# Kernel optimization log

Measured on AMD Instinct MI355X. Metric: run time of the kernel, lower is better.

## Reference

```python
import jax, jax.numpy as jnp
import numpy as np

EMBED = 2048
HEAD = 128

def setup_inputs() -> dict:
    key = jax.random.key(0)
    ks = jax.random.split(key, 7)
    s = 1.0 / np.sqrt(EMBED)
    x = jax.random.normal(ks[0], (8, 2048, EMBED), dtype=jnp.float32)
    Wq = jax.random.uniform(ks[1], (EMBED, HEAD), jnp.float32, -s, s)
    bq = jax.random.uniform(ks[2], (HEAD,), jnp.float32, -s, s)
    Wk = jax.random.uniform(ks[3], (EMBED, HEAD), jnp.float32, -s, s)
    bk = jax.random.uniform(ks[4], (HEAD,), jnp.float32, -s, s)
    Wv = jax.random.uniform(ks[5], (EMBED, HEAD), jnp.float32, -s, s)
    bv = jax.random.uniform(ks[6], (HEAD,), jnp.float32, -s, s)
    return {"x": x, "Wq": Wq, "bq": bq, "Wk": Wk, "bk": bk, "Wv": Wv, "bv": bv}

def reference(x, Wq, bq, Wk, bk, Wv, bv):
    # x: [B, T, E]
    T = x.shape[1]
    Q = x @ Wq + bq  # [B, T, H]
    K = x @ Wk + bk
    V = x @ Wv + bv
    scale = 1.0 / jnp.sqrt(jnp.float32(HEAD))
    scores = jnp.einsum('bqh,bkh->bqk', Q, K) * scale  # [B, T, T]
    causal = jnp.tril(jnp.ones((T, T), dtype=bool))
    scores = jnp.where(causal, scores, jnp.float32(-jnp.inf))
    att = jax.nn.softmax(scores, axis=-1)
    # dropout is identity in eval/reference mode
    return jnp.einsum('bqk,bkh->bqh', att, V)
```

## Files before the change

### kernel.cpp

```cpp
#include <hip/hip_runtime.h>

#define EMBED 2048
#define HEAD 128
#define BATCH 8
#define SEQ 2048

typedef __attribute__((ext_vector_type(4))) float f32x4;
typedef __attribute__((ext_vector_type(8))) __bf16 bf16x8;
typedef __attribute__((ext_vector_type(8))) short short8;

static __device__ __forceinline__ ushort f2bf(float x){
    unsigned u = __float_as_uint(x);
    u += 0x7fffu + ((u >> 16) & 1u);
    return (ushort)(u >> 16);
}

#define MFMA16(a,b,c) __builtin_amdgcn_mfma_f32_16x16x32_bf16((a),(b),(c),0,0,0)

#define GLL16(g, l) __builtin_amdgcn_global_load_lds( \
    (const __attribute__((address_space(1))) void*)(g), \
    (__attribute__((address_space(3))) void*)(l), 16, 0, 0)

__global__ __launch_bounds__(256) void prep_wt(const float* __restrict__ Wq,
                                               const float* __restrict__ Wk,
                                               const float* __restrict__ Wv,
                                               ushort* __restrict__ wt){
    __shared__ float ld[64][129];
    const int w  = blockIdx.y;
    const int k0 = blockIdx.x * 64;
    const int tid = threadIdx.x;
    const float* W = (w == 0) ? Wq : ((w == 1) ? Wk : Wv);
    #pragma unroll
    for (int ii = 0; ii < 32; ii++){
        int idx = tid + 256 * ii;
        int row = idx >> 7, col = idx & 127;
        ld[row][col] = W[(size_t)(k0 + row) * HEAD + col];
    }
    __syncthreads();
    int n  = tid >> 1;
    int kh = (tid & 1) * 32;
    __attribute__((aligned(16))) ushort tmp[32];
    #pragma unroll
    for (int ii = 0; ii < 32; ii++) tmp[ii] = f2bf(ld[kh + ii][n]);
    ushort* dst = wt + (size_t)(w * HEAD + n) * EMBED + k0 + kh;
    #pragma unroll
    for (int q = 0; q < 4; q++)
        *(short8*)(dst + q * 8) = *(const short8*)(tmp + q * 8);
}

__global__ __launch_bounds__(256) void qkv_gemm(const float* __restrict__ x,
                                                const ushort* __restrict__ wt,
                                                const float* __restrict__ bq,
                                                const float* __restrict__ bk,
                                                const float* __restrict__ bv,
                                                ushort* __restrict__ Qb,
                                                ushort* __restrict__ Kb,
                                                ushort* __restrict__ Vt){
    __shared__ char smem[51200];
    float* ts = (float*)smem;

    const int nt    = blockIdx.x;
    const int mtile = blockIdx.y;
    const int tid   = threadIdx.x;
    const int lane  = tid & 63;
    const int wid   = tid >> 6;
    const int l15   = lane & 15, lhi = lane >> 4;
    const int wm    = wid >> 1,  wn  = wid & 1;
    const int xrow0 = mtile * 64;

    const int srow = tid >> 3;
    const int ssub = tid & 7;

    const ushort* wtn = wt + (size_t)(nt * HEAD) * EMBED;
    const int grow = lane >> 3;
    const int gch  = lane & 7;

    f32x4 acc[2][4];
    #pragma unroll
    for (int i = 0; i < 2; i++)
        #pragma unroll
        for (int j = 0; j < 4; j++) acc[i][j] = (f32x4){0.f,0.f,0.f,0.f};

    float4 xr[2][2];
    const int NK = EMBED / 64;

    {
        const float* xp = x + (size_t)xrow0 * EMBED;
        #pragma unroll
        for (int h = 0; h < 2; h++){
            xr[h][0] = *(const float4*)(xp + (size_t)(srow + 32*h) * EMBED + ssub * 8);
            xr[h][1] = *(const float4*)(xp + (size_t)(srow + 32*h) * EMBED + ssub * 8 + 4);
        }
        #pragma unroll
        for (int g = 0; g < 4; g++){
            int r0  = wid * 32 + g * 8;
            int row = r0 + grow;
            GLL16(wtn + (size_t)row * EMBED + ((gch ^ grow) * 8), smem + 18432 + r0 * 128);
        }
        #pragma unroll
        for (int h = 0; h < 2; h++){
            __attribute__((aligned(16))) ushort t8[8];
            t8[0]=f2bf(xr[h][0].x); t8[1]=f2bf(xr[h][0].y); t8[2]=f2bf(xr[h][0].z); t8[3]=f2bf(xr[h][0].w);
            t8[4]=f2bf(xr[h][1].x); t8[5]=f2bf(xr[h][1].y); t8[6]=f2bf(xr[h][1].z); t8[7]=f2bf(xr[h][1].w);
            *(short8*)(smem + (srow + 32*h) * 144 + ssub * 16) = *(const short8*)t8;
        }
    }
    __syncthreads();

    int cur = 0;
    for (int kt = 0; kt < NK; ++kt){
        char* xsb_c = smem + cur * 9216;
        char* wlb_c = smem + 18432 + cur * 16384;
        char* xsb_n = smem + (cur ^ 1) * 9216;
        char* wlb_n = smem + 18432 + (cur ^ 1) * 16384;
        if (kt < NK - 1){
            const float* xp = x + (size_t)xrow0 * EMBED + (kt + 1) * 64;
            #pragma unroll
            for (int h = 0; h < 2; h++){
                xr[h][0] = *(const float4*)(xp + (size_t)(srow + 32*h) * EMBED + ssub * 8);
                xr[h][1] = *(const float4*)(xp + (size_t)(srow + 32*h) * EMBED + ssub * 8 + 4);
            }
            const ushort* wsrc = wtn + (kt + 1) * 64;
            #pragma unroll
            for (int g = 0; g < 4; g++){
                int r0  = wid * 32 + g * 8;
                int row = r0 + grow;
                GLL16(wsrc + (size_t)row * EMBED + ((gch ^ grow) * 8), wlb_n + r0 * 128);
            }
        }
        #pragma unroll
        for (int kc = 0; kc < 2; kc++){
            bf16x8 af[2], bfj[4];
            #pragma unroll
            for (int i = 0; i < 2; i++)
                af[i] = *(const bf16x8*)(xsb_c + (wm*32 + i*16 + l15) * 144 + kc*64 + lhi*16);
            #pragma unroll
            for (int j = 0; j < 4; j++){
                int row = wn*64 + j*16 + l15;
                bfj[j] = *(const bf16x8*)(wlb_c + row * 128 + (((kc*4 + lhi) ^ (l15 & 7)) * 16));
            }
            #pragma unroll
            for (int i = 0; i < 2; i++)
                #pragma unroll
                for (int j = 0; j < 4; j++)
                    acc[i][j] = MFMA16(af[i], bfj[j], acc[i][j]);
        }
        if (kt < NK - 1){
            #pragma unroll
            for (int h = 0; h < 2; h++){
                __attribute__((aligned(16))) ushort t8[8];
                t8[0]=f2bf(xr[h][0].x); t8[1]=f2bf(xr[h][0].y); t8[2]=f2bf(xr[h][0].z); t8[3]=f2bf(xr[h][0].w);
                t8[4]=f2bf(xr[h][1].x); t8[5]=f2bf(xr[h][1].y); t8[6]=f2bf(xr[h][1].z); t8[7]=f2bf(xr[h][1].w);
                *(short8*)(xsb_n + (srow + 32*h) * 144 + ssub * 16) = *(const short8*)t8;
            }
        }
        __syncthreads();
        cur ^= 1;
    }

    const float* bias = (nt == 0) ? bq : ((nt == 1) ? bk : bv);
    float bval[4];
    #pragma unroll
    for (int j = 0; j < 4; j++) bval[j] = bias[wn*64 + j*16 + l15];

    if (nt < 2){
        ushort* dst = (nt == 0) ? Qb : Kb;
        #pragma unroll
        for (int i = 0; i < 2; i++)
            #pragma unroll
            for (int j = 0; j < 4; j++)
                #pragma unroll
                for (int r = 0; r < 4; r++){
                    int m = mtile*64 + wm*32 + i*16 + lhi*4 + r;
                    int c = wn*64 + j*16 + l15;
                    dst[(size_t)m * HEAD + c] = f2bf(acc[i][j][r] + bval[j]);
                }
    } else {
        __syncthreads();
        #pragma unroll
        for (int i = 0; i < 2; i++)
            #pragma unroll
            for (int j = 0; j < 4; j++)
                #pragma unroll
                for (int r = 0; r < 4; r++){
                    int ml = wm*32 + i*16 + lhi*4 + r;
                    int c  = wn*64 + j*16 + l15;
                    ts[ml * 132 + c] = acc[i][j][r] + bval[j];
                }
        __syncthreads();
        int n  = tid >> 1;
        int mc = (tid & 1) * 32;
        int bb = mtile >> 5;
        int trow = (mtile & 31) * 64 + mc;
        __attribute__((aligned(16))) ushort tmp[32];
        #pragma unroll
        for (int ii = 0; ii < 32; ii++) tmp[ii] = f2bf(ts[(mc + ii) * 132 + n]);
        ushort* dst = Vt + ((size_t)(bb * HEAD + n)) * SEQ + trow;
        #pragma unroll
        for (int q = 0; q < 4; q++)
            *(short8*)(dst + q * 8) = *(const short8*)(tmp + q * 8);
    }
}

__global__ __launch_bounds__(256) void attn(const ushort* __restrict__ Qb,
                                            const ushort* __restrict__ Kb,
                                            const ushort* __restrict__ Vt,
                                            float* __restrict__ po,
                                            float* __restrict__ pm,
                                            float* __restrict__ pl){
    __shared__ char smem[40960];
    char* Ks = smem;
    char* Vs = smem + 16384;
    char* Ps = smem + 32768;

    const int slot = blockIdx.x;
    const int b    = blockIdx.y;
    const int qi   = slot >> 1;
    const int qt   = (b < 4) ? qi : (31 - qi);
    const int half = slot & 1;
    const int NT   = qt + 1;
    const int tmid = (NT + 1) >> 1;
    const int t0   = half ? tmid : 0;
    const int t1   = half ? NT : tmid;

    const int qb    = qt * 64;
    const int tid   = threadIdx.x;
    const int lane  = tid & 63, wid = tid >> 6;
    const int l15   = lane & 15, lhi = lane >> 4;
    const float scale = 0.08838834764831845f;

    bf16x8 qf[4];
    {
        const ushort* qp = Qb + ((size_t)(b * SEQ + qb + wid * 16 + l15)) * HEAD;
        #pragma unroll
        for (int kc = 0; kc < 4; kc++)
            qf[kc] = *(const bf16x8*)(qp + kc * 32 + lhi * 8);
    }

    f32x4 o[8];
    #pragma unroll
    for (int d = 0; d < 8; d++) o[d] = (f32x4){0.f,0.f,0.f,0.f};
    float mr[4] = {-1e30f,-1e30f,-1e30f,-1e30f};
    float lr[4] = {0.f,0.f,0.f,0.f};

    char* Pw = Ps + wid * 2048;

    const int krow = tid >> 4, kch = tid & 15;
    const int vd   = tid >> 3, vch = tid & 7;

    short8 kr[4], vr[4];
    {
        const int kvb = t0 * 64;
        #pragma unroll
        for (int j = 0; j < 4; j++)
            kr[j] = *(const short8*)(Kb + ((size_t)(b * SEQ + kvb + krow + 16*j)) * HEAD + kch * 8);
        #pragma unroll
        for (int j = 0; j < 4; j++)
            vr[j] = *(const short8*)(Vt + ((size_t)(b * HEAD + vd + 32*j)) * SEQ + kvb + vch * 8);
    }

    for (int t = t0; t < t1; ++t){
        __syncthreads();
        #pragma unroll
        for (int j = 0; j < 4; j++){
            int row = krow + 16*j;
            *(short8*)(Ks + row * 256 + ((kch ^ (row & 15)) * 16)) = kr[j];
        }
        #pragma unroll
        for (int j = 0; j < 4; j++){
            int d = vd + 32*j;
            *(short8*)(Vs + d * 128 + ((vch ^ (d & 7)) * 16)) = vr[j];
        }
        if (t + 1 < t1){
            const int kvb2 = (t + 1) * 64;
            #pragma unroll
            for (int j = 0; j < 4; j++)
                kr[j] = *(const short8*)(Kb + ((size_t)(b * SEQ + kvb2 + krow + 16*j)) * HEAD + kch * 8);
            #pragma unroll
            for (int j = 0; j < 4; j++)
                vr[j] = *(const short8*)(Vt + ((size_t)(b * HEAD + vd + 32*j)) * SEQ + kvb2 + vch * 8);
        }
        asm volatile("s_waitcnt lgkmcnt(0)" ::: "memory");
        __builtin_amdgcn_s_barrier();
        __builtin_amdgcn_sched_barrier(0);

        const int kvb = t * 64;
        f32x4 s[4];
        #pragma unroll
        for (int ns = 0; ns < 4; ns++){
            s[ns] = (f32x4){0.f,0.f,0.f,0.f};
            int row = ns * 16 + l15;
            #pragma unroll
            for (int kc = 0; kc < 4; kc++){
                int ch = (kc * 4 + lhi) ^ (row & 15);
                bf16x8 bfr = *(const bf16x8*)(Ks + row * 256 + ch * 16);
                s[ns] = MFMA16(qf[kc], bfr, s[ns]);
            }
        }

        float mx[4];
        #pragma unroll
        for (int r = 0; r < 4; r++){
            #pragma unroll
            for (int ns = 0; ns < 4; ns++){
                float v = s[ns][r] * scale;
                if (t == qt){
                    int kvg = kvb + ns * 16 + l15;
                    int qg  = qb + wid * 16 + lhi * 4 + r;
                    if (kvg > qg) v = -1e30f;
                }
                s[ns][r] = v;
            }
            float m0 = fmaxf(fmaxf(s[0][r], s[1][r]), fmaxf(s[2][r], s[3][r]));
            m0 = fmaxf(m0, __shfl_xor(m0, 1));
            m0 = fmaxf(m0, __shfl_xor(m0, 2));
            m0 = fmaxf(m0, __shfl_xor(m0, 4));
            m0 = fmaxf(m0, __shfl_xor(m0, 8));
            mx[r] = m0;
        }
        float alpha[4];
        #pragma unroll
        for (int r = 0; r < 4; r++){
            float mn = fmaxf(mr[r], mx[r]);
            alpha[r] = __expf(mr[r] - mn);
            mr[r] = mn;
            float sum = 0.f;
            #pragma unroll
            for (int ns = 0; ns < 4; ns++){
                float p = __expf(s[ns][r] - mn);
                s[ns][r] = p;
                sum += p;
            }
            sum += __shfl_xor(sum, 1);
            sum += __shfl_xor(sum, 2);
            sum += __shfl_xor(sum, 4);
            sum += __shfl_xor(sum, 8);
            lr[r] = lr[r] * alpha[r] + sum;
        }
        #pragma unroll
        for (int d = 0; d < 8; d++)
            #pragma unroll
            for (int r = 0; r < 4; r++) o[d][r] *= alpha[r];

        #pragma unroll
        for (int ns = 0; ns < 4; ns++)
            #pragma unroll
            for (int r = 0; r < 4; r++){
                int row = lhi * 4 + r;
                int byteoff = row * 128 + (((ns * 16 + l15) * 2) ^ ((row & 7) << 4));
                *(ushort*)(Pw + byteoff) = f2bf(s[ns][r]);
            }
        asm volatile("s_waitcnt lgkmcnt(0)" ::: "memory");
        __builtin_amdgcn_sched_barrier(0);

        #pragma unroll
        for (int kc = 0; kc < 2; kc++){
            int abyte = l15 * 128 + ((kc * 64 + lhi * 16) ^ ((l15 & 7) << 4));
            bf16x8 af = *(const bf16x8*)(Pw + abyte);
            #pragma unroll
            for (int ds = 0; ds < 8; ds++){
                int drow = ds * 16 + l15;
                int bbyte = drow * 128 + ((kc * 64 + lhi * 16) ^ ((drow & 7) << 4));
                bf16x8 bfr = *(const bf16x8*)(Vs + bbyte);
                o[ds] = MFMA16(af, bfr, o[ds]);
            }
        }
    }

    float* pob = po + ((size_t)half * 16384 + (size_t)b * SEQ) * HEAD;
    #pragma unroll
    for (int r = 0; r < 4; r++){
        int q = qb + wid * 16 + lhi * 4 + r;
        #pragma unroll
        for (int ds = 0; ds < 8; ds++)
            pob[(size_t)q * HEAD + ds * 16 + l15] = o[ds][r];
        if (l15 == 0){
            pm[half * 16384 + b * SEQ + q] = mr[r];
            pl[half * 16384 + b * SEQ + q] = lr[r];
        }
    }
}

__global__ __launch_bounds__(256) void merge(const float* __restrict__ po,
                                             const float* __restrict__ pm,
                                             const float* __restrict__ pl,
                                             float* __restrict__ out){
    int g = blockIdx.x * 256 + threadIdx.x;
    int row = g >> 2;
    int dq  = (g & 3) * 32;
    float m0 = pm[row], m1 = pm[16384 + row];
    float l0 = pl[row], l1 = pl[16384 + row];
    float M  = fmaxf(m0, m1);
    float w0 = __expf(m0 - M), w1 = __expf(m1 - M);
    float inv = 1.0f / (w0 * l0 + w1 * l1);
    const float4* p0 = (const float4*)(po + (size_t)row * HEAD + dq);
    const float4* p1 = (const float4*)(po + (size_t)(16384 + row) * HEAD + dq);
    float4* op = (float4*)(out + (size_t)row * HEAD + dq);
    #pragma unroll
    for (int i = 0; i < 8; i++){
        float4 a = p0[i], c = p1[i];
        float4 r;
        r.x = (w0*a.x + w1*c.x) * inv;
        r.y = (w0*a.y + w1*c.y) * inv;
        r.z = (w0*a.z + w1*c.z) * inv;
        r.w = (w0*a.w + w1*c.w) * inv;
        op[i] = r;
    }
}

extern "C" void kernel_launch(void* const* d_in, const int* in_sizes, int n_in,
                              void* d_out, int out_size, void* d_ws, size_t ws_size,
                              hipStream_t stream){
    const float* x  = (const float*)d_in[0];
    const float* Wq = (const float*)d_in[1];
    const float* bq = (const float*)d_in[2];
    const float* Wk = (const float*)d_in[3];
    const float* bk = (const float*)d_in[4];
    const float* Wv = (const float*)d_in[5];
    const float* bv = (const float*)d_in[6];
    float* out = (float*)d_out;

    char* ws = (char*)d_ws;
    ushort* Qb = (ushort*)ws;
    ushort* Kb = (ushort*)(ws + (size_t)4  * 1024 * 1024);
    ushort* Vt = (ushort*)(ws + (size_t)8  * 1024 * 1024);
    ushort* Wt = (ushort*)(ws + (size_t)12 * 1024 * 1024);
    float*  po = (float*) (ws + (size_t)14 * 1024 * 1024);
    float*  pm = (float*) (ws + (size_t)31 * 1024 * 1024);
    float*  pl = (float*) (ws + (size_t)31 * 1024 * 1024 + 262144);

    prep_wt <<<dim3(32, 3), 256, 0, stream>>>(Wq, Wk, Wv, Wt);
    qkv_gemm<<<dim3(3, 256), 256, 0, stream>>>(x, Wt, bq, bk, bv, Qb, Kb, Vt);
    attn    <<<dim3(64, 8), 256, 0, stream>>>(Qb, Kb, Vt, po, pm, pl);
    merge   <<<256, 256, 0, stream>>>(po, pm, pl, out);
}
```

Measured before the change: 115.0 us.

## Fuse Q/K/V projections into one block per row tile to read x once

Each QKV GEMM block now computes all 384 output columns (Q, K and V) for its 64-row tile, using 512 threads and 8 waves laid out 2x4, instead of launching three blocks per tile that each reload and re-convert the same x rows. This cuts the fp32 x global traffic and the bf16 conversion work by a factor of three. In exchange, LDS use grows to about 114 KB per block, which limits occupancy, and only 256 blocks are launched, which may underfill the GPU. The epilogue routes the column groups to Q, K or the transposed V buffer.

```diff
diff --git a/kernel.cpp b/kernel.cpp
--- a/kernel.cpp
+++ b/kernel.cpp
@@ -48,7 +48,7 @@
         *(short8*)(dst + q * 8) = *(const short8*)(tmp + q * 8);
 }
 
-__global__ __launch_bounds__(256) void qkv_gemm(const float* __restrict__ x,
+__global__ __launch_bounds__(512) void qkv_gemm(const float* __restrict__ x,
                                                 const ushort* __restrict__ wt,
                                                 const float* __restrict__ bq,
                                                 const float* __restrict__ bk,
@@ -56,149 +56,136 @@
                                                 ushort* __restrict__ Qb,
                                                 ushort* __restrict__ Kb,
                                                 ushort* __restrict__ Vt){
-    __shared__ char smem[51200];
+    __shared__ char smem[116736];
     float* ts = (float*)smem;
 
-    const int nt    = blockIdx.x;
-    const int mtile = blockIdx.y;
+    const int mtile = blockIdx.x;
     const int tid   = threadIdx.x;
     const int lane  = tid & 63;
     const int wid   = tid >> 6;
     const int l15   = lane & 15, lhi = lane >> 4;
-    const int wm    = wid >> 1,  wn  = wid & 1;
+    const int wm    = wid >> 2,  wn  = wid & 3;
     const int xrow0 = mtile * 64;
 
     const int srow = tid >> 3;
     const int ssub = tid & 7;
 
-    const ushort* wtn = wt + (size_t)(nt * HEAD) * EMBED;
     const int grow = lane >> 3;
     const int gch  = lane & 7;
 
-    f32x4 acc[2][4];
+    f32x4 acc[2][6];
     #pragma unroll
     for (int i = 0; i < 2; i++)
         #pragma unroll
-        for (int j = 0; j < 4; j++) acc[i][j] = (f32x4){0.f,0.f,0.f,0.f};
-
-    float4 xr[2][2];
+        for (int j = 0; j < 6; j++) acc[i][j] = (f32x4){0.f,0.f,0.f,0.f};
+
+    float4 xr0, xr1;
     const int NK = EMBED / 64;
 
     {
-        const float* xp = x + (size_t)xrow0 * EMBED;
-        #pragma unroll
-        for (int h = 0; h < 2; h++){
-            xr[h][0] = *(const float4*)(xp + (size_t)(srow + 32*h) * EMBED + ssub * 8);
-            xr[h][1] = *(const float4*)(xp + (size_t)(srow + 32*h) * EMBED + ssub * 8 + 4);
-        }
-        #pragma unroll
-        for (int g = 0; g < 4; g++){
-            int r0  = wid * 32 + g * 8;
+        const float* xp = x + (size_t)(xrow0 + srow) * EMBED;
+        xr0 = *(const float4*)(xp + ssub * 8);
+        xr1 = *(const float4*)(xp + ssub * 8 + 4);
+        #pragma unroll
+        for (int g = 0; g < 6; g++){
+            int r0  = wid * 48 + g * 8;
             int row = r0 + grow;
-            GLL16(wtn + (size_t)row * EMBED + ((gch ^ grow) * 8), smem + 18432 + r0 * 128);
-        }
-        #pragma unroll
-        for (int h = 0; h < 2; h++){
-            __attribute__((aligned(16))) ushort t8[8];
-            t8[0]=f2bf(xr[h][0].x); t8[1]=f2bf(xr[h][0].y); t8[2]=f2bf(xr[h][0].z); t8[3]=f2bf(xr[h][0].w);
-            t8[4]=f2bf(xr[h][1].x); t8[5]=f2bf(xr[h][1].y); t8[6]=f2bf(xr[h][1].z); t8[7]=f2bf(xr[h][1].w);
-            *(short8*)(smem + (srow + 32*h) * 144 + ssub * 16) = *(const short8*)t8;
-        }
+            GLL16(wt + (size_t)row * EMBED + ((gch ^ grow) * 8), smem + 18432 + r0 * 128);
+        }
+        __attribute__((aligned(16))) ushort t8[8];
+        t8[0]=f2bf(xr0.x); t8[1]=f2bf(xr0.y); t8[2]=f2bf(xr0.z); t8[3]=f2bf(xr0.w);
+        t8[4]=f2bf(xr1.x); t8[5]=f2bf(xr1.y); t8[6]=f2bf(xr1.z); t8[7]=f2bf(xr1.w);
+        *(short8*)(smem + srow * 144 + ssub * 16) = *(const short8*)t8;
     }
     __syncthreads();
 
     int cur = 0;
     for (int kt = 0; kt < NK; ++kt){
         char* xsb_c = smem + cur * 9216;
-        char* wlb_c = smem + 18432 + cur * 16384;
+        char* wlb_c = smem + 18432 + cur * 49152;
         char* xsb_n = smem + (cur ^ 1) * 9216;
-        char* wlb_n = smem + 18432 + (cur ^ 1) * 16384;
+        char* wlb_n = smem + 18432 + (cur ^ 1) * 49152;
         if (kt < NK - 1){
-            const float* xp = x + (size_t)xrow0 * EMBED + (kt + 1) * 64;
-            #pragma unroll
-            for (int h = 0; h < 2; h++){
-                xr[h][0] = *(const float4*)(xp + (size_t)(srow + 32*h) * EMBED + ssub * 8);
-                xr[h][1] = *(const float4*)(xp + (size_t)(srow + 32*h) * EMBED + ssub * 8 + 4);
-            }
-            const ushort* wsrc = wtn + (kt + 1) * 64;
-            #pragma unroll
-            for (int g = 0; g < 4; g++){
-                int r0  = wid * 32 + g * 8;
+            const float* xp = x + (size_t)(xrow0 + srow) * EMBED + (kt + 1) * 64;
+            xr0 = *(const float4*)(xp + ssub * 8);
+            xr1 = *(const float4*)(xp + ssub * 8 + 4);
+            const ushort* wsrc = wt + (kt + 1) * 64;
+            #pragma unroll
+            for (int g = 0; g < 6; g++){
+                int r0  = wid * 48 + g * 8;
                 int row = r0 + grow;
                 GLL16(wsrc + (size_t)row * EMBED + ((gch ^ grow) * 8), wlb_n + r0 * 128);
             }
         }
         #pragma unroll
         for (int kc = 0; kc < 2; kc++){
-            bf16x8 af[2], bfj[4];
+            bf16x8 af[2], bfj[6];
             #pragma unroll
             for (int i = 0; i < 2; i++)
                 af[i] = *(const bf16x8*)(xsb_c + (wm*32 + i*16 + l15) * 144 + kc*64 + lhi*16);
             #pragma unroll
-            for (int j = 0; j < 4; j++){
-                int row = wn*64 + j*16 + l15;
+            for (int j = 0; j < 6; j++){
+                int row = wn*96 + j*16 + l15;
                 bfj[j] = *(const bf16x8*)(wlb_c + row * 128 + (((kc*4 + lhi) ^ (l15 & 7)) * 16));
             }
             #pragma unroll
             for (int i = 0; i < 2; i++)
                 #pragma unroll
-                for (int j = 0; j < 4; j++)
+                for (int j = 0; j < 6; j++)
                     acc[i][j] = MFMA16(af[i], bfj[j], acc[i][j]);
         }
         if (kt < NK - 1){
-            #pragma unroll
-            for (int h = 0; h < 2; h++){
-                __attribute__((aligned(16))) ushort t8[8];
-                t8[0]=f2bf(xr[h][0].x); t8[1]=f2bf(xr[h][0].y); t8[2]=f2bf(xr[h][0].z); t8[3]=f2bf(xr[h][0].w);
-                t8[4]=f2bf(xr[h][1].x); t8[5]=f2bf(xr[h][1].y); t8[6]=f2bf(xr[h][1].z); t8[7]=f2bf(xr[h][1].w);
-                *(short8*)(xsb_n + (srow + 32*h) * 144 + ssub * 16) = *(const short8*)t8;
-            }
+            __attribute__((aligned(16))) ushort t8[8];
+            t8[0]=f2bf(xr0.x); t8[1]=f2bf(xr0.y); t8[2]=f2bf(xr0.z); t8[3]=f2bf(xr0.w);
+            t8[4]=f2bf(xr1.x); t8[5]=f2bf(xr1.y); t8[6]=f2bf(xr1.z); t8[7]=f2bf(xr1.w);
+            *(short8*)(xsb_n + srow * 144 + ssub * 16) = *(const short8*)t8;
         }
         __syncthreads();
         cur ^= 1;
     }
 
-    const float* bias = (nt == 0) ? bq : ((nt == 1) ? bk : bv);
-    float bval[4];
-    #pragma unroll
-    for (int j = 0; j < 4; j++) bval[j] = bias[wn*64 + j*16 + l15];
-
-    if (nt < 2){
-        ushort* dst = (nt == 0) ? Qb : Kb;
-        #pragma unroll
-        for (int i = 0; i < 2; i++)
-            #pragma unroll
-            for (int j = 0; j < 4; j++)
+    float bval[6];
+    #pragma unroll
+    for (int j = 0; j < 6; j++){
+        int c = wn*96 + j*16 + l15;
+        bval[j] = (c < 128) ? bq[c] : ((c < 256) ? bk[c - 128] : bv[c - 256]);
+    }
+    #pragma unroll
+    for (int j = 0; j < 6; j++){
+        int cb = wn*96 + j*16;
+        if (cb < 256){
+            ushort* dst = (cb < 128) ? Qb : Kb;
+            int cl = (cb & 127) + l15;
+            #pragma unroll
+            for (int i = 0; i < 2; i++)
                 #pragma unroll
                 for (int r = 0; r < 4; r++){
                     int m = mtile*64 + wm*32 + i*16 + lhi*4 + r;
-                    int c = wn*64 + j*16 + l15;
-                    dst[(size_t)m * HEAD + c] = f2bf(acc[i][j][r] + bval[j]);
+                    dst[(size_t)m * HEAD + cl] = f2bf(acc[i][j][r] + bval[j]);
                 }
-    } else {
-        __syncthreads();
-        #pragma unroll
-        for (int i = 0; i < 2; i++)
-            #pragma unroll
-            for (int j = 0; j < 4; j++)
+        } else {
+            int vc = cb - 256 + l15;
+            #pragma unroll
+            for (int i = 0; i < 2; i++)
                 #pragma unroll
                 for (int r = 0; r < 4; r++){
                     int ml = wm*32 + i*16 + lhi*4 + r;
-                    int c  = wn*64 + j*16 + l15;
-                    ts[ml * 132 + c] = acc[i][j][r] + bval[j];
+                    ts[ml * 132 + vc] = acc[i][j][r] + bval[j];
                 }
-        __syncthreads();
-        int n  = tid >> 1;
-        int mc = (tid & 1) * 32;
+        }
+    }
+    __syncthreads();
+    {
+        int n  = tid >> 2;
+        int mc = (tid & 3) * 16;
         int bb = mtile >> 5;
         int trow = (mtile & 31) * 64 + mc;
-        __attribute__((aligned(16))) ushort tmp[32];
-        #pragma unroll
-        for (int ii = 0; ii < 32; ii++) tmp[ii] = f2bf(ts[(mc + ii) * 132 + n]);
+        __attribute__((aligned(16))) ushort tmp[16];
+        #pragma unroll
+        for (int ii = 0; ii < 16; ii++) tmp[ii] = f2bf(ts[(mc + ii) * 132 + n]);
         ushort* dst = Vt + ((size_t)(bb * HEAD + n)) * SEQ + trow;
-        #pragma unroll
-        for (int q = 0; q < 4; q++)
-            *(short8*)(dst + q * 8) = *(const short8*)(tmp + q * 8);
+        *(short8*)(dst)     = *(const short8*)(tmp);
+        *(short8*)(dst + 8) = *(const short8*)(tmp + 8);
     }
 }
 
@@ -430,7 +417,7 @@
     float*  pl = (float*) (ws + (size_t)31 * 1024 * 1024 + 262144);
 
     prep_wt <<<dim3(32, 3), 256, 0, stream>>>(Wq, Wk, Wv, Wt);
-    qkv_gemm<<<dim3(3, 256), 256, 0, stream>>>(x, Wt, bq, bk, bv, Qb, Kb, Vt);
+    qkv_gemm<<<dim3(256), 512, 0, stream>>>(x, Wt, bq, bk, bv, Qb, Kb, Vt);
     attn    <<<dim3(64, 8), 256, 0, stream>>>(Qb, Kb, Vt, po, pm, pl);
     merge   <<<256, 256, 0, stream>>>(po, pm, pl, out);
 }
```

Result: faster. 99.09 us (-13.8%).
